# Kernel optimization log

Measured on AMD Instinct MI355X. Metric: run time of the kernel, lower is better.

The kernel has to match this reference:

```python
import jax, jax.numpy as jnp
import numpy as np

B, T, D = 4, 2048, 1024
H, Dh = 16, 64


def setup_inputs() -> dict:
    key = jax.random.key(0)
    ks = jax.random.split(key, 5)
    # kaiming_normal_ on [H, Dh, D]: fan_in = Dh*D (torch default fan_in over dims[1:]),
    # std = sqrt(2/fan_in); exact init distribution does not affect correctness checks.
    std_qkv = float(np.sqrt(2.0 / (Dh * D)))
    std_o = float(np.sqrt(2.0 / (D * Dh)))
    return {
        "x": jax.random.normal(ks[0], (B, T, D), dtype=jnp.float32),
        "W_Q": jax.random.normal(ks[1], (H, Dh, D), dtype=jnp.float32) * std_qkv,
        "b_Q": jnp.zeros((H, Dh), dtype=jnp.float32),
        "W_K": jax.random.normal(ks[2], (H, Dh, D), dtype=jnp.float32) * std_qkv,
        "b_K": jnp.zeros((H, Dh), dtype=jnp.float32),
        "W_V": jax.random.normal(ks[3], (H, Dh, D), dtype=jnp.float32) * std_qkv,
        "b_V": jnp.zeros((H, Dh), dtype=jnp.float32),
        "W_O": jax.random.normal(ks[4], (H, D, Dh), dtype=jnp.float32) * std_o,
        "b_O": jnp.zeros((D,), dtype=jnp.float32),
    }


def reference(x, W_Q, b_Q, W_K, b_K, W_V, b_V, W_O, b_O):
    # Q/K/V: [batch, tok, heads, d_head]
    Q = jnp.einsum("btd,hkd->bthk", x, W_Q) + b_Q
    K = jnp.einsum("btd,hkd->bthk", x, W_K) + b_K
    V = jnp.einsum("btd,hkd->bthk", x, W_V) + b_V
    d_head = W_Q.shape[1]
    # scores: [batch, heads, tok_Q, tok_K]
    scores = jnp.einsum("bqhk,bshk->bhqs", Q, K) / jnp.sqrt(jnp.asarray(d_head, x.dtype))
    attn = jax.nn.softmax(scores, axis=-1)
    # out per head: [batch, tok_Q, heads, d_head]
    out_h = jnp.einsum("bhqs,bshk->bqhk", attn, V)
    # project back: [batch, tok, d_model]
    return jnp.einsum("bqhk,hdk->bqd", out_h, W_O) + b_O
```

## Files before the change

### kernel.cpp

```cpp
#include <hip/hip_runtime.h>
#include <stdint.h>


typedef __attribute__((ext_vector_type(8))) short bf16x8;
typedef __attribute__((ext_vector_type(4))) float f32x4;

#define MFMA32 __builtin_amdgcn_mfma_f32_16x16x32_bf16

#if __has_builtin(__builtin_amdgcn_exp2f)
#define EXP2(x) __builtin_amdgcn_exp2f(x)
#else
#define EXP2(x) exp2f(x)
#endif

__device__ __forceinline__ unsigned short f2bf(float f) {
  union { float f; unsigned int u; } v; v.f = f;
  unsigned int r = v.u + 0x7FFFu + ((v.u >> 16) & 1u);
  return (unsigned short)(r >> 16);
}

__device__ __forceinline__ void gl_lds16(const void* g, void* l) {
  __builtin_amdgcn_global_load_lds(
      (const __attribute__((address_space(1))) unsigned int*)g,
      (__attribute__((address_space(3))) unsigned int*)l, 16, 0, 0);
}

__device__ __forceinline__ unsigned packbf2(float lo, float hi) {
  union { float f; unsigned u; } a, b; a.f = lo; b.f = hi;
  return __builtin_amdgcn_perm(b.u, a.u, 0x07060302u);
}

__device__ __forceinline__ int rho(int r) { return (r & 3) | ((r >> 1) & 4); }

__device__ __forceinline__ void conv8(const float* __restrict__ src,
                                      unsigned short* __restrict__ dst, int i) {
  const float4* sp = (const float4*)src;
  float4 a = sp[2 * i], b = sp[2 * i + 1];
  union { unsigned short u[8]; uint4 v; } o;
  o.u[0] = f2bf(a.x); o.u[1] = f2bf(a.y); o.u[2] = f2bf(a.z); o.u[3] = f2bf(a.w);
  o.u[4] = f2bf(b.x); o.u[5] = f2bf(b.y); o.u[6] = f2bf(b.z); o.u[7] = f2bf(b.w);
  ((uint4*)dst)[i] = o.v;
}

__global__ __launch_bounds__(256) void prep_all(
    const float* __restrict__ x, const float* __restrict__ WQ,
    const float* __restrict__ WK, const float* __restrict__ WV,
    const float* __restrict__ WO, unsigned short* __restrict__ Xb,
    unsigned short* __restrict__ Wqkv, unsigned short* __restrict__ Wot) {
  const int bx = blockIdx.x, t = threadIdx.x;
  if (bx < 4096) {
    conv8(x, Xb, bx * 256 + t);
  } else if (bx < 4608) {
    conv8(WQ, Wqkv, (bx - 4096) * 256 + t);
  } else if (bx < 5120) {
    conv8(WK, Wqkv + 1048576, (bx - 4608) * 256 + t);
  } else if (bx < 5632) {
    conv8(WV, Wqkv + 2097152, (bx - 5120) * 256 + t);
  } else {
    int tid = (bx - 5632) * 256 + t;
    int h = tid >> 13, rem = tid & 8191;
    int d = rem >> 3, c = rem & 7;
    const float4* sp = (const float4*)(WO + (size_t)h * 65536 + d * 64 + c * 8);
    float4 a = sp[0], e = sp[1];
    union { unsigned short u[8]; uint4 v; } o;
    o.u[0] = f2bf(a.x); o.u[1] = f2bf(a.y); o.u[2] = f2bf(a.z); o.u[3] = f2bf(a.w);
    o.u[4] = f2bf(e.x); o.u[5] = f2bf(e.y); o.u[6] = f2bf(e.z); o.u[7] = f2bf(e.w);
    *(uint4*)(Wot + (size_t)d * 1024 + h * 64 + c * 8) = o.v;
  }
}

__device__ __forceinline__ void gemm_mainloop_1024(
    const unsigned short* __restrict__ A, const unsigned short* __restrict__ B,
    unsigned short* As, unsigned short* Bs, int m0, int n0, f32x4 acc[4][4]) {
  const int tid = threadIdx.x;
  const int lane = tid & 63, w = tid >> 6;
  const int quad = lane >> 4, l15 = lane & 15;
  const int wm = w & 1, wn = w >> 1;
  int srow[4], scl[4];
#pragma unroll
  for (int u = 0; u < 4; ++u) {
    int s = u * 256 + tid;
    srow[u] = s >> 3;
    scl[u] = ((s & 7) ^ ((s >> 3) & 7)) * 8;
  }
  for (int k0 = 0; k0 < 1024; k0 += 64) {
    __syncthreads();
#pragma unroll
    for (int u = 0; u < 4; ++u) {
      int s = u * 256 + tid;
      gl_lds16(A + (size_t)(m0 + srow[u]) * 1024 + k0 + scl[u], As + s * 8);
      gl_lds16(B + (size_t)(n0 + srow[u]) * 1024 + k0 + scl[u], Bs + s * 8);
    }
    __syncthreads();
    bf16x8 af[4][2], bfr[4][2];
#pragma unroll
    for (int i = 0; i < 4; ++i) {
      int ra = wm * 64 + i * 16 + l15;
      int rb = wn * 64 + i * 16 + l15;
#pragma unroll
      for (int c = 0; c < 2; ++c) {
        af[i][c]  = *(const bf16x8*)(As + ra * 64 + (((c * 4 + quad) ^ (ra & 7)) * 8));
        bfr[i][c] = *(const bf16x8*)(Bs + rb * 64 + (((c * 4 + quad) ^ (rb & 7)) * 8));
      }
    }
#pragma unroll
    for (int mi = 0; mi < 4; ++mi)
#pragma unroll
      for (int nj = 0; nj < 4; ++nj) {
        acc[mi][nj] = MFMA32(af[mi][0], bfr[nj][0], acc[mi][nj], 0, 0, 0);
        acc[mi][nj] = MFMA32(af[mi][1], bfr[nj][1], acc[mi][nj], 0, 0, 0);
      }
  }
}

__global__ __launch_bounds__(256) void gemm_qkv(
    const unsigned short* __restrict__ Xb, const unsigned short* __restrict__ Wqkv,
    const float* __restrict__ bQ, const float* __restrict__ bK,
    const float* __restrict__ bV, unsigned short* __restrict__ Qg,
    unsigned short* __restrict__ Kg, unsigned int* __restrict__ Vpg) {
  __shared__ unsigned short As[128 * 64];
  __shared__ unsigned short Bs[128 * 64];
  const int tid = threadIdx.x, lane = tid & 63, w = tid >> 6;
  const int quad = lane >> 4, l15 = lane & 15;
  const int wm = w & 1, wn = w >> 1;
  const int m0 = blockIdx.x * 128, n0 = blockIdx.y * 128;
  f32x4 acc[4][4];
#pragma unroll
  for (int i = 0; i < 4; ++i)
#pragma unroll
    for (int j = 0; j < 4; ++j) acc[i][j] = (f32x4){0.f, 0.f, 0.f, 0.f};

  gemm_mainloop_1024(Xb, Wqkv, As, Bs, m0, n0, acc);

  const int type = n0 >> 10;
  const int nreg = n0 & 1023;
  const float* bias = (type == 0) ? bQ : (type == 1) ? bK : bV;
#pragma unroll
  for (int nj = 0; nj < 4; ++nj) {
    const int n_loc = nreg + wn * 64 + nj * 16 + l15;
    const int h = n_loc >> 6, kh = n_loc & 63;
    const float bv = bias[n_loc];
#pragma unroll
    for (int mi = 0; mi < 4; ++mi) {
      const int mb = m0 + wm * 64 + mi * 16 + quad * 4;
      const int b = mb >> 11, tb = mb & 2047;
      if (type == 2) {
        uint2 pk;
        pk.x = (unsigned)f2bf(acc[mi][nj][0] + bv) |
               ((unsigned)f2bf(acc[mi][nj][1] + bv) << 16);
        pk.y = (unsigned)f2bf(acc[mi][nj][2] + bv) |
               ((unsigned)f2bf(acc[mi][nj][3] + bv) << 16);
        *(uint2*)(Vpg + ((size_t)(b * 16 + h) * 64 + kh) * 1024 + (tb >> 1)) = pk;
      } else {
        unsigned short* dst =
            ((type == 0) ? Qg : Kg) + ((size_t)(b * 16 + h) * 2048 + tb) * 64 + kh;
        const float sc = (type == 0) ? 0.18033688011112042f : 1.0f;
        dst[0]   = f2bf((acc[mi][nj][0] + bv) * sc);
        dst[64]  = f2bf((acc[mi][nj][1] + bv) * sc);
        dst[128] = f2bf((acc[mi][nj][2] + bv) * sc);
        dst[192] = f2bf((acc[mi][nj][3] + bv) * sc);
      }
    }
  }
}

__device__ __forceinline__ void stage_kv(const unsigned short* __restrict__ Kb,
                                         const unsigned int* __restrict__ Vb,
                                         unsigned short* smem, int tid, int s0, int b) {
#pragma unroll
  for (int u = 0; u < 2; ++u) {
    int s = u * 256 + tid, row = s >> 3, g = (s & 7) ^ rho(row);
    gl_lds16(Kb + (size_t)(s0 + row) * 64 + g * 8, smem + b * 8192 + s * 8);
    gl_lds16(Vb + (size_t)row * 1024 + (s0 >> 1) + g * 4,
             smem + b * 8192 + 4096 + s * 8);
  }
}

__global__ __launch_bounds__(256, 4) void flash_attn(
    const unsigned short* __restrict__ Qg, const unsigned short* __restrict__ Kg,
    const unsigned int* __restrict__ Vpg, unsigned short* __restrict__ OH) {
  __shared__ unsigned short smem[16384];
  const int tid = threadIdx.x, lane = tid & 63, w = tid >> 6;
  const int quad = lane >> 4, l15 = lane & 15;
  const int qt = blockIdx.x, bh = blockIdx.y;

  const unsigned short* Qb = Qg + ((size_t)bh * 2048 + qt * 128) * 64;
  const unsigned short* Kb = Kg + (size_t)bh * 2048 * 64;
  const unsigned int*  Vb = Vpg + (size_t)bh * 64 * 1024;

#pragma unroll
  for (int u = 0; u < 4; ++u) {
    int s = u * 256 + tid, row = s >> 3;
    gl_lds16(Qb + row * 64 + ((s & 7) ^ (row & 7)) * 8, smem + s * 8);
  }
  __syncthreads();

  bf16x8 qf[2][2];
#pragma unroll
  for (int qi = 0; qi < 2; ++qi) {
    int row = w * 32 + qi * 16 + l15;
#pragma unroll
    for (int c = 0; c < 2; ++c)
      qf[qi][c] = *(const bf16x8*)(smem + row * 64 + (((c * 4 + quad) ^ (row & 7)) * 8));
  }
  __syncthreads();

  stage_kv(Kb, Vb, smem, tid, 0, 0);

  f32x4 o[2][4];
  float l_part[2] = {0.f, 0.f};
#pragma unroll
  for (int qi = 0; qi < 2; ++qi)
#pragma unroll
    for (int nj = 0; nj < 4; ++nj) o[qi][nj] = (f32x4){0.f, 0.f, 0.f, 0.f};

  for (int t = 0; t < 32; ++t) {
    __syncthreads();
    if (t < 31) stage_kv(Kb, Vb, smem, tid, (t + 1) * 64, (t + 1) & 1);
    const unsigned short* Kd = smem + (t & 1) * 8192;
    const unsigned short* Vd = Kd + 4096;

#pragma unroll
    for (int blk = 0; blk < 2; ++blk) {
      bf16x8 vb[4];
#pragma unroll
      for (int nj = 0; nj < 4; ++nj) {
        int vrow = nj * 16 + l15;
        vb[nj] = *(const bf16x8*)(Vd + vrow * 64 + (((blk * 4 + quad) ^ rho(vrow)) * 8));
      }
      union { unsigned u[4]; bf16x8 v; } pa0, pa1;
#pragma unroll
      for (int v = 0; v < 2; ++v) {
        int krow = blk * 32 + 8 * (l15 >> 2) + 4 * v + (l15 & 3);
        const unsigned short* kr = Kd + krow * 64;
        bf16x8 ka0 = *(const bf16x8*)(kr + ((quad ^ rho(krow)) * 8));
        bf16x8 ka1 = *(const bf16x8*)(kr + (((4 + quad) ^ rho(krow)) * 8));
        f32x4 S0 = (f32x4){0.f, 0.f, 0.f, 0.f}, S1 = S0;
        S0 = MFMA32(ka0, qf[0][0], S0, 0, 0, 0);
        S0 = MFMA32(ka1, qf[0][1], S0, 0, 0, 0);
        S1 = MFMA32(ka0, qf[1][0], S1, 0, 0, 0);
        S1 = MFMA32(ka1, qf[1][1], S1, 0, 0, 0);
        float e0 = EXP2(S0[0]), e1 = EXP2(S0[1]), e2 = EXP2(S0[2]), e3 = EXP2(S0[3]);
        float f0 = EXP2(S1[0]), f1 = EXP2(S1[1]), f2 = EXP2(S1[2]), f3 = EXP2(S1[3]);
        l_part[0] += (e0 + e1) + (e2 + e3);
        l_part[1] += (f0 + f1) + (f2 + f3);
        pa0.u[2 * v] = packbf2(e0, e1); pa0.u[2 * v + 1] = packbf2(e2, e3);
        pa1.u[2 * v] = packbf2(f0, f1); pa1.u[2 * v + 1] = packbf2(f2, f3);
      }
#pragma unroll
      for (int nj = 0; nj < 4; ++nj) {
        o[0][nj] = MFMA32(pa0.v, vb[nj], o[0][nj], 0, 0, 0);
        o[1][nj] = MFMA32(pa1.v, vb[nj], o[1][nj], 0, 0, 0);
      }
    }
  }

  const int b = bh >> 4, h = bh & 15;
#pragma unroll
  for (int qi = 0; qi < 2; ++qi) {
    float l = l_part[qi];
    l += __shfl_xor(l, 16);
    l += __shfl_xor(l, 32);
    float linv = 1.0f / l;
#pragma unroll
    for (int r = 0; r < 4; ++r) {
      float lr = __shfl(linv, 4 * quad + r);
      int trow = qt * 128 + w * 32 + qi * 16 + 4 * quad + r;
#pragma unroll
      for (int nj = 0; nj < 4; ++nj) {
        int col = h * 64 + nj * 16 + l15;
        OH[((size_t)b * 2048 + trow) * 1024 + col] = f2bf(o[qi][nj][r] * lr);
      }
    }
  }
}

__global__ __launch_bounds__(256) void gemm_o(
    const unsigned short* __restrict__ OHm, const unsigned short* __restrict__ Wot,
    const float* __restrict__ bO, float* __restrict__ Out) {
  __shared__ unsigned short As[128 * 64];
  __shared__ unsigned short Bs[128 * 64];
  const int tid = threadIdx.x, lane = tid & 63, w = tid >> 6;
  const int quad = lane >> 4, l15 = lane & 15;
  const int wm = w & 1, wn = w >> 1;
  const int m0 = blockIdx.x * 128, n0 = blockIdx.y * 128;
  f32x4 acc[4][4];
#pragma unroll
  for (int i = 0; i < 4; ++i)
#pragma unroll
    for (int j = 0; j < 4; ++j) acc[i][j] = (f32x4){0.f, 0.f, 0.f, 0.f};

  gemm_mainloop_1024(OHm, Wot, As, Bs, m0, n0, acc);

#pragma unroll
  for (int nj = 0; nj < 4; ++nj) {
    const int n = n0 + wn * 64 + nj * 16 + l15;
    const float bv = bO[n];
#pragma unroll
    for (int mi = 0; mi < 4; ++mi) {
      const int mb = m0 + wm * 64 + mi * 16 + quad * 4;
#pragma unroll
      for (int r = 0; r < 4; ++r)
        Out[(size_t)(mb + r) * 1024 + n] = acc[mi][nj][r] + bv;
    }
  }
}

extern "C" void kernel_launch(void* const* d_in, const int* in_sizes, int n_in,
                              void* d_out, int out_size, void* d_ws, size_t ws_size,
                              hipStream_t stream) {
  const float* x  = (const float*)d_in[0];
  const float* WQ = (const float*)d_in[1];
  const float* bQ = (const float*)d_in[2];
  const float* WK = (const float*)d_in[3];
  const float* bK = (const float*)d_in[4];
  const float* WV = (const float*)d_in[5];
  const float* bV = (const float*)d_in[6];
  const float* WO = (const float*)d_in[7];
  const float* bO = (const float*)d_in[8];
  float* out = (float*)d_out;

  char* ws = (char*)d_ws;
  unsigned short* Xb   = (unsigned short*)(ws);
  unsigned short* OH   = (unsigned short*)(ws);
  unsigned short* Wqkv = (unsigned short*)(ws + 16777216);
  unsigned short* Wot  = (unsigned short*)(ws + 23068672);
  unsigned short* Qg   = (unsigned short*)(ws + 25165824);
  unsigned short* Kg   = (unsigned short*)(ws + 41943040);
  unsigned int*   Vpg  = (unsigned int*)  (ws + 58720256);

  prep_all<<<6144, 256, 0, stream>>>(x, WQ, WK, WV, WO, Xb, Wqkv, Wot);

  dim3 g1(64, 24);
  gemm_qkv<<<g1, 256, 0, stream>>>(Xb, Wqkv, bQ, bK, bV, Qg, Kg, Vpg);
  dim3 g2(16, 64);
  flash_attn<<<g2, 256, 0, stream>>>(Qg, Kg, Vpg, OH);
  dim3 g3(64, 8);
  gemm_o<<<g3, 256, 0, stream>>>(OH, Wot, bO, out);
}
```

Before: 288.9 us.

## Double flash-attention query tile to 256 rows per block for more K/V reuse

Each flash-attention block now handles 256 query rows instead of 128, so every wave keeps four 16-row Q fragments and four output accumulators. Each K/V tile staged in LDS is reused across twice as many queries, halving total K/V global traffic and staging overhead. The grid is halved to 512 blocks, occupancy bounds drop to 2 for attention, and gemm_qkv gets a min-blocks hint of 5. The trade-offs are higher register pressure and fewer blocks to spread over the CUs.

```diff
diff --git a/kernel.cpp b/kernel.cpp
--- a/kernel.cpp
+++ b/kernel.cpp
@@ -113,7 +113,7 @@
   }
 }
 
-__global__ __launch_bounds__(256) void gemm_qkv(
+__global__ __launch_bounds__(256, 5) void gemm_qkv(
     const unsigned short* __restrict__ Xb, const unsigned short* __restrict__ Wqkv,
     const float* __restrict__ bQ, const float* __restrict__ bK,
     const float* __restrict__ bV, unsigned short* __restrict__ Qg,
@@ -176,7 +176,7 @@
   }
 }
 
-__global__ __launch_bounds__(256, 4) void flash_attn(
+__global__ __launch_bounds__(256, 2) void flash_attn(
     const unsigned short* __restrict__ Qg, const unsigned short* __restrict__ Kg,
     const unsigned int* __restrict__ Vpg, unsigned short* __restrict__ OH) {
   __shared__ unsigned short smem[16384];
@@ -184,21 +184,21 @@
   const int quad = lane >> 4, l15 = lane & 15;
   const int qt = blockIdx.x, bh = blockIdx.y;
 
-  const unsigned short* Qb = Qg + ((size_t)bh * 2048 + qt * 128) * 64;
+  const unsigned short* Qb = Qg + ((size_t)bh * 2048 + qt * 256) * 64;
   const unsigned short* Kb = Kg + (size_t)bh * 2048 * 64;
   const unsigned int*  Vb = Vpg + (size_t)bh * 64 * 1024;
 
 #pragma unroll
-  for (int u = 0; u < 4; ++u) {
+  for (int u = 0; u < 8; ++u) {
     int s = u * 256 + tid, row = s >> 3;
     gl_lds16(Qb + row * 64 + ((s & 7) ^ (row & 7)) * 8, smem + s * 8);
   }
   __syncthreads();
 
-  bf16x8 qf[2][2];
-#pragma unroll
-  for (int qi = 0; qi < 2; ++qi) {
-    int row = w * 32 + qi * 16 + l15;
+  bf16x8 qf[4][2];
+#pragma unroll
+  for (int qi = 0; qi < 4; ++qi) {
+    int row = w * 64 + qi * 16 + l15;
 #pragma unroll
     for (int c = 0; c < 2; ++c)
       qf[qi][c] = *(const bf16x8*)(smem + row * 64 + (((c * 4 + quad) ^ (row & 7)) * 8));
@@ -207,10 +207,10 @@
 
   stage_kv(Kb, Vb, smem, tid, 0, 0);
 
-  f32x4 o[2][4];
-  float l_part[2] = {0.f, 0.f};
-#pragma unroll
-  for (int qi = 0; qi < 2; ++qi)
+  f32x4 o[4][4];
+  float l_part[4] = {0.f, 0.f, 0.f, 0.f};
+#pragma unroll
+  for (int qi = 0; qi < 4; ++qi)
 #pragma unroll
     for (int nj = 0; nj < 4; ++nj) o[qi][nj] = (f32x4){0.f, 0.f, 0.f, 0.f};
 
@@ -228,36 +228,35 @@
         int vrow = nj * 16 + l15;
         vb[nj] = *(const bf16x8*)(Vd + vrow * 64 + (((blk * 4 + quad) ^ rho(vrow)) * 8));
       }
-      union { unsigned u[4]; bf16x8 v; } pa0, pa1;
+      union { unsigned u[4]; bf16x8 v; } pa[4];
 #pragma unroll
       for (int v = 0; v < 2; ++v) {
         int krow = blk * 32 + 8 * (l15 >> 2) + 4 * v + (l15 & 3);
         const unsigned short* kr = Kd + krow * 64;
         bf16x8 ka0 = *(const bf16x8*)(kr + ((quad ^ rho(krow)) * 8));
         bf16x8 ka1 = *(const bf16x8*)(kr + (((4 + quad) ^ rho(krow)) * 8));
-        f32x4 S0 = (f32x4){0.f, 0.f, 0.f, 0.f}, S1 = S0;
-        S0 = MFMA32(ka0, qf[0][0], S0, 0, 0, 0);
-        S0 = MFMA32(ka1, qf[0][1], S0, 0, 0, 0);
-        S1 = MFMA32(ka0, qf[1][0], S1, 0, 0, 0);
-        S1 = MFMA32(ka1, qf[1][1], S1, 0, 0, 0);
-        float e0 = EXP2(S0[0]), e1 = EXP2(S0[1]), e2 = EXP2(S0[2]), e3 = EXP2(S0[3]);
-        float f0 = EXP2(S1[0]), f1 = EXP2(S1[1]), f2 = EXP2(S1[2]), f3 = EXP2(S1[3]);
-        l_part[0] += (e0 + e1) + (e2 + e3);
-        l_part[1] += (f0 + f1) + (f2 + f3);
-        pa0.u[2 * v] = packbf2(e0, e1); pa0.u[2 * v + 1] = packbf2(e2, e3);
-        pa1.u[2 * v] = packbf2(f0, f1); pa1.u[2 * v + 1] = packbf2(f2, f3);
-      }
-#pragma unroll
-      for (int nj = 0; nj < 4; ++nj) {
-        o[0][nj] = MFMA32(pa0.v, vb[nj], o[0][nj], 0, 0, 0);
-        o[1][nj] = MFMA32(pa1.v, vb[nj], o[1][nj], 0, 0, 0);
-      }
+#pragma unroll
+        for (int qi = 0; qi < 4; ++qi) {
+          f32x4 S = (f32x4){0.f, 0.f, 0.f, 0.f};
+          S = MFMA32(ka0, qf[qi][0], S, 0, 0, 0);
+          S = MFMA32(ka1, qf[qi][1], S, 0, 0, 0);
+          float e0 = EXP2(S[0]), e1 = EXP2(S[1]), e2 = EXP2(S[2]), e3 = EXP2(S[3]);
+          l_part[qi] += (e0 + e1) + (e2 + e3);
+          pa[qi].u[2 * v] = packbf2(e0, e1);
+          pa[qi].u[2 * v + 1] = packbf2(e2, e3);
+        }
+      }
+#pragma unroll
+      for (int nj = 0; nj < 4; ++nj)
+#pragma unroll
+        for (int qi = 0; qi < 4; ++qi)
+          o[qi][nj] = MFMA32(pa[qi].v, vb[nj], o[qi][nj], 0, 0, 0);
     }
   }
 
   const int b = bh >> 4, h = bh & 15;
 #pragma unroll
-  for (int qi = 0; qi < 2; ++qi) {
+  for (int qi = 0; qi < 4; ++qi) {
     float l = l_part[qi];
     l += __shfl_xor(l, 16);
     l += __shfl_xor(l, 32);
@@ -265,7 +264,7 @@
 #pragma unroll
     for (int r = 0; r < 4; ++r) {
       float lr = __shfl(linv, 4 * quad + r);
-      int trow = qt * 128 + w * 32 + qi * 16 + 4 * quad + r;
+      int trow = qt * 256 + w * 64 + qi * 16 + 4 * quad + r;
 #pragma unroll
       for (int nj = 0; nj < 4; ++nj) {
         int col = h * 64 + nj * 16 + l15;
@@ -333,7 +332,7 @@
 
   dim3 g1(64, 24);
   gemm_qkv<<<g1, 256, 0, stream>>>(Xb, Wqkv, bQ, bK, bV, Qg, Kg, Vpg);
-  dim3 g2(16, 64);
+  dim3 g2(8, 64);
   flash_attn<<<g2, 256, 0, stream>>>(Qg, Kg, Vpg, OH);
   dim3 g3(64, 8);
   gemm_o<<<g3, 256, 0, stream>>>(OH, Wot, bO, out);
```

Result: slower. 306.9 us (+6.2%).
